# Kernel tuning notes

Hardware: AMD Instinct MI355X
Metric: run time of the kernel (lower is better)

Reference implementation:

```python
import jax, jax.numpy as jnp
import numpy as np

N, E, M, H, D, G, C = 50000, 400000, 4, 400, 3, 128, 10
BN_EPS = 1e-5


def setup_inputs() -> dict:
    key = jax.random.key(0)
    ks = iter(jax.random.split(key, 64))

    def rn(shape, s=0.05):
        return (jax.random.normal(next(ks), shape, jnp.float32) * s)

    inp = {}
    inp['x'] = jax.random.normal(next(ks), (N, M), jnp.float32)
    inp['edge_index'] = jax.random.randint(next(ks), (2, E), 0, N, dtype=jnp.int32)
    inp['batch'] = jnp.sort(jax.random.randint(next(ks), (N,), 0, G, dtype=jnp.int32))
    inp['num_graphs'] = G
    # first GINConv MLP: M -> H -> H -> H
    inp['c0_w1'] = rn((H, M)); inp['c0_b1'] = rn((H,))
    inp['c0_g1'] = jnp.ones((H,), jnp.float32); inp['c0_be1'] = jnp.zeros((H,), jnp.float32)
    inp['c0_w2'] = rn((H, H)); inp['c0_b2'] = rn((H,))
    inp['c0_g2'] = jnp.ones((H,), jnp.float32); inp['c0_be2'] = jnp.zeros((H,), jnp.float32)
    inp['c0_w3'] = rn((H, H)); inp['c0_b3'] = rn((H,))
    # GINConv layers 1..D-1 (stacked): H -> H -> H -> H
    L = D - 1
    inp['cw1'] = rn((L, H, H)); inp['cb1'] = rn((L, H))
    inp['cg1'] = jnp.ones((L, H), jnp.float32); inp['cbe1'] = jnp.zeros((L, H), jnp.float32)
    inp['cw2'] = rn((L, H, H)); inp['cb2'] = rn((L, H))
    inp['cg2'] = jnp.ones((L, H), jnp.float32); inp['cbe2'] = jnp.zeros((L, H), jnp.float32)
    inp['cw3'] = rn((L, H, H)); inp['cb3'] = rn((L, H))
    # readout head
    inp['lin1_w'] = rn((H * D // 2, H * D)); inp['lin1_b'] = rn((H * D // 2,))
    inp['lin2_w'] = rn((C, H * D // 2)); inp['lin2_b'] = rn((C,))
    return inp


def _bn(z, g, b):
    # training-mode BatchNorm1d over nodes (biased variance, eps=1e-5)
    m = z.mean(axis=0)
    v = ((z - m) ** 2).mean(axis=0)
    return (z - m) * jax.lax.rsqrt(v + BN_EPS) * g + b


def _mlp(h, w1, b1, g1, be1, w2, b2, g2, be2, w3, b3):
    # PyG MLP(num_layers=3): Lin->BN->ReLU, Lin->BN->ReLU, Lin (plain last)
    h = jax.nn.relu(_bn(h @ w1.T + b1, g1, be1))
    h = jax.nn.relu(_bn(h @ w2.T + b2, g2, be2))
    return h @ w3.T + b3


def reference(x, edge_index, batch, num_graphs,
              c0_w1, c0_b1, c0_g1, c0_be1, c0_w2, c0_b2, c0_g2, c0_be2, c0_w3, c0_b3,
              cw1, cb1, cg1, cbe1, cw2, cb2, cg2, cbe2, cw3, cb3,
              lin1_w, lin1_b, lin2_w, lin2_b):
    src, dst = edge_index[0], edge_index[1]
    n = x.shape[0]

    def gin_agg(h):
        # eps = -1.0 => (1+eps)*x_i term vanishes; pure neighbor scatter-add
        return jax.ops.segment_sum(h[src], dst, num_segments=n)

    pools = []
    h = _mlp(gin_agg(x), c0_w1, c0_b1, c0_g1, c0_be1,
             c0_w2, c0_b2, c0_g2, c0_be2, c0_w3, c0_b3)
    pools.append(jax.ops.segment_sum(h, batch, num_segments=num_graphs))
    for i in range(D - 1):
        h = _mlp(gin_agg(h), cw1[i], cb1[i], cg1[i], cbe1[i],
                 cw2[i], cb2[i], cg2[i], cbe2[i], cw3[i], cb3[i])
        pools.append(jax.ops.segment_sum(h, batch, num_segments=num_graphs))
    xG = jnp.concatenate(pools, axis=1)                 # [G, D*H]
    z = jax.nn.relu(xG @ lin1_w.T + lin1_b)             # dropout off (eval)
    z = z @ lin2_w.T + lin2_b
    return jax.nn.log_softmax(z, axis=1)
```

## Files before the change

### kernel.cpp

```cpp
#include <hip/hip_runtime.h>
#include <hip/hip_bf16.h>
#include <math.h>
#include <cstdint>

static constexpr int NN = 50000;
static constexpr int NE = 400000;
static constexpr int H  = 400;
static constexpr int NG = 128;
static constexpr int NC = 10;
static constexpr float EPS = 1e-5f;
static constexpr int NB1 = (NN + 255) / 256;
static constexpr int KP  = 416;
static constexpr int SREP = 8;
static constexpr int SSLOT = SREP * 2 * KP;

typedef unsigned short u16;
typedef __attribute__((ext_vector_type(8))) unsigned short u16x8;
typedef __attribute__((ext_vector_type(4))) unsigned short u16x4;
typedef __attribute__((ext_vector_type(8))) short bf16x8;
typedef __attribute__((ext_vector_type(4))) float f32x4;

__device__ __forceinline__ float bf2f(u16 u) {
    return __uint_as_float(((uint32_t)u) << 16);
}
__device__ __forceinline__ u16 f2bf(float f) {
    uint32_t u = __float_as_uint(f);
    return (u16)((u + 0x7FFFu + ((u >> 16) & 1u)) >> 16);
}
__device__ __forceinline__ void gload_lds16(const void* g, void* lds) {
    __builtin_amdgcn_global_load_lds((const __attribute__((address_space(1))) void*)g,
                                     (__attribute__((address_space(3))) void*)lds, 16, 0, 0);
}

__device__ __forceinline__ bf16x8 bnrelu8(bf16x8 a, const float* __restrict__ scp,
                                          const float* __restrict__ shp) {
    union { bf16x8 v; uint32_t u[4]; } in, out;
    in.v = a;
#pragma unroll
    for (int p = 0; p < 4; ++p) {
        float lo = __uint_as_float(in.u[p] << 16);
        float hi = __uint_as_float(in.u[p] & 0xFFFF0000u);
        lo = fmaxf(fmaf(lo, scp[2 * p], shp[2 * p]), 0.f);
        hi = fmaxf(fmaf(hi, scp[2 * p + 1], shp[2 * p + 1]), 0.f);
        asm("v_cvt_pk_bf16_f32 %0, %1, %2" : "=v"(out.u[p]) : "v"(lo), "v"(hi));
    }
    return out.v;
}


__global__ void k_count(const int* __restrict__ dst, int* __restrict__ deg) {
    int e = blockIdx.x * blockDim.x + threadIdx.x;
    if (e < NE) atomicAdd(&deg[dst[e]], 1);
}

__global__ __launch_bounds__(256) void k_scan1(const int* __restrict__ deg,
                                               int* __restrict__ part,
                                               int* __restrict__ btot) {
    __shared__ int sd[256];
    int t = threadIdx.x;
    int i = blockIdx.x * 256 + t;
    int v = (i < NN) ? deg[i] : 0;
    sd[t] = v;
    __syncthreads();
#pragma unroll
    for (int off = 1; off < 256; off <<= 1) {
        int x = (t >= off) ? sd[t - off] : 0;
        __syncthreads();
        sd[t] += x;
        __syncthreads();
    }
    if (i < NN) part[i] = sd[t];
    if (t == 255) btot[blockIdx.x] = sd[255];
}

__global__ __launch_bounds__(256) void k_scan2(int* __restrict__ btot) {
    __shared__ int sd[256];
    int t = threadIdx.x;
    int v = (t < NB1) ? btot[t] : 0;
    sd[t] = v;
    __syncthreads();
#pragma unroll
    for (int off = 1; off < 256; off <<= 1) {
        int x = (t >= off) ? sd[t - off] : 0;
        __syncthreads();
        sd[t] += x;
        __syncthreads();
    }
    if (t < NB1) btot[t] = sd[t];
}

__global__ __launch_bounds__(256) void k_scan3(const int* __restrict__ part,
                                               const int* __restrict__ btot,
                                               const int* __restrict__ deg,
                                               int* __restrict__ rowp,
                                               int* __restrict__ cur) {
    int i = blockIdx.x * 256 + threadIdx.x;
    if (i < NN) {
        int s = part[i] + (blockIdx.x ? btot[blockIdx.x - 1] : 0);
        rowp[i + 1] = s;
        cur[i] = s - deg[i];
    }
    if (i == 0) rowp[0] = 0;
}

__global__ void k_scatter(const int* __restrict__ src, const int* __restrict__ dst,
                          int* __restrict__ cur, int* __restrict__ csrc) {
    int e = blockIdx.x * blockDim.x + threadIdx.x;
    if (e < NE) {
        int d = dst[e];
        int p = atomicAdd(&cur[d], 1);
        csrc[p] = src[e];
    }
}


__global__ __launch_bounds__(256) void k_cntg(const int* __restrict__ batch,
                                              int* __restrict__ cnt) {
    __shared__ int hh[NG];
    int t = threadIdx.x;
    for (int i = t; i < NG; i += 256) hh[i] = 0;
    __syncthreads();
    int n = blockIdx.x * 256 + t;
    if (n < NN) atomicAdd(&hh[batch[n]], 1);
    __syncthreads();
    for (int i = t; i < NG; i += 256)
        if (hh[i]) atomicAdd(&cnt[i], hh[i]);
}


__global__ void k_cvtw3(const float* __restrict__ s0, const float* __restrict__ s1,
                        const float* __restrict__ s2, u16* __restrict__ dst) {
    int i = blockIdx.x * blockDim.x + threadIdx.x;
    if (i >= 3 * 400 * 52) return;
    int rc = i / 52;
    int c8 = (i % 52) * 8;
    u16x8 o = {0, 0, 0, 0, 0, 0, 0, 0};
    if (c8 < 400) {
        int mat = rc / 400, row = rc % 400;
        const float* s = (mat == 0 ? s0 : mat == 1 ? s1 : s2) + (long)row * 400;
        float4 a = *(const float4*)(s + c8);
        float4 b = *(const float4*)(s + c8 + 4);
        o[0] = f2bf(a.x); o[1] = f2bf(a.y); o[2] = f2bf(a.z); o[3] = f2bf(a.w);
        o[4] = f2bf(b.x); o[5] = f2bf(b.y); o[6] = f2bf(b.z); o[7] = f2bf(b.w);
    }
    *(u16x8*)(dst + (long)rc * KP + c8) = o;
}


__global__ __launch_bounds__(256) void k_wmerge(const float* __restrict__ Wa,
                                                const float* __restrict__ Wb,
                                                u16* __restrict__ dst) {
    __shared__ float As[16][68];
    __shared__ float Bs[16][68];
    const int bc = blockIdx.x * 64, bj = blockIdx.y * 64;
    const int t = threadIdx.x;
    const int tx = t & 15, ty = t >> 4;
    float acc[4][4] = {};
    for (int k0 = 0; k0 < 400; k0 += 16) {
        {
            int c = bc + (t >> 2);
            int kq = (t & 3) * 4;
            float4 v = make_float4(0.f, 0.f, 0.f, 0.f);
            if (c < 400) v = *(const float4*)(Wa + (long)c * 400 + k0 + kq);
            As[kq + 0][t >> 2] = v.x; As[kq + 1][t >> 2] = v.y;
            As[kq + 2][t >> 2] = v.z; As[kq + 3][t >> 2] = v.w;
        }
        {
            int k = k0 + (t >> 4);
            int jq = (t & 15) * 4;
            int j = bj + jq;
            float4 v = make_float4(0.f, 0.f, 0.f, 0.f);
            if (j < 400) v = *(const float4*)(Wb + (long)k * 400 + j);
            Bs[t >> 4][jq + 0] = v.x; Bs[t >> 4][jq + 1] = v.y;
            Bs[t >> 4][jq + 2] = v.z; Bs[t >> 4][jq + 3] = v.w;
        }
        __syncthreads();
#pragma unroll
        for (int kk = 0; kk < 16; ++kk) {
            float4 av = *(const float4*)&As[kk][ty * 4];
            float4 bv = *(const float4*)&Bs[kk][tx * 4];
            float a[4] = {av.x, av.y, av.z, av.w};
            float b[4] = {bv.x, bv.y, bv.z, bv.w};
#pragma unroll
            for (int i = 0; i < 4; ++i)
#pragma unroll
                for (int j = 0; j < 4; ++j)
                    acc[i][j] = fmaf(a[i], b[j], acc[i][j]);
        }
        __syncthreads();
    }
#pragma unroll
    for (int i = 0; i < 4; ++i) {
        int c = bc + ty * 4 + i;
        if (c >= 400) continue;
#pragma unroll
        for (int j = 0; j < 4; ++j) {
            int col = bj + tx * 4 + j;
            if (col < KP) dst[(long)c * KP + col] = (col < 400) ? f2bf(acc[i][j]) : 0;
        }
    }
}

__global__ void k_wbias(const float* __restrict__ Wa, const float* __restrict__ b,
                        float* __restrict__ bb) {
    int c = blockIdx.x * blockDim.x + threadIdx.x;
    if (c >= 400) return;
    const float4* wr = (const float4*)(Wa + (long)c * 400);
    const float4* br = (const float4*)b;
    float s0 = 0.f, s1 = 0.f, s2 = 0.f, s3 = 0.f;
    for (int q = 0; q < 100; ++q) {
        float4 a = wr[q], v = br[q];
        s0 = fmaf(a.x, v.x, s0); s1 = fmaf(a.y, v.y, s1);
        s2 = fmaf(a.z, v.z, s2); s3 = fmaf(a.w, v.w, s3);
    }
    bb[c] = s0 + s1 + s2 + s3;
}


__global__ void k_agg0(const float* __restrict__ x, const int* __restrict__ rowp,
                       const int* __restrict__ csrc, float* __restrict__ out) {
    int n = blockIdx.x * blockDim.x + threadIdx.x;
    if (n >= NN) return;
    float4 acc = make_float4(0.f, 0.f, 0.f, 0.f);
    int b = rowp[n], e = rowp[n + 1];
    for (int p = b; p < e; ++p) {
        float4 v = ((const float4*)x)[csrc[p]];
        acc.x += v.x; acc.y += v.y; acc.z += v.z; acc.w += v.w;
    }
    ((float4*)out)[n] = acc;
}

__global__ __launch_bounds__(256) void k_aggH(const u16* __restrict__ h,
                                              const int* __restrict__ rowp,
                                              const int* __restrict__ csrc,
                                              const float* __restrict__ bias,
                                              u16* __restrict__ out) {
    int n = (blockIdx.x << 2) + (threadIdx.x >> 6);
    if (n >= NN) return;
    int l = threadIdx.x & 63;
    if (l >= 50) return;
    float4 b0 = *(const float4*)(bias + l * 8);
    float4 b1 = *(const float4*)(bias + l * 8 + 4);
    float acc[8] = {b0.x, b0.y, b0.z, b0.w, b1.x, b1.y, b1.z, b1.w};
    int b = rowp[n], e = rowp[n + 1];
    for (int p = b; p < e; ++p) {
        const u16* r = h + (long)csrc[p] * H + l * 8;
        u16x8 v = *(const u16x8*)r;
#pragma unroll
        for (int q = 0; q < 8; ++q) acc[q] += bf2f(v[q]);
    }
    u16x8 o;
#pragma unroll
    for (int q = 0; q < 8; ++q) o[q] = f2bf(acc[q]);
    *(u16x8*)(out + (long)n * H + l * 8) = o;
}


__global__ void k_lin0(const float* __restrict__ a4, const float* __restrict__ w,
                       const float* __restrict__ b, u16* __restrict__ out) {
    long i = (long)blockIdx.x * blockDim.x + threadIdx.x;
    if (i >= (long)NN * 100) return;
    int n = (int)(i / 100), q = (int)(i - (long)n * 100);
    int j0 = q * 4;
    float4 av = ((const float4*)a4)[n];
    u16x4 o;
#pragma unroll
    for (int jj = 0; jj < 4; ++jj) {
        float4 wv = ((const float4*)w)[j0 + jj];
        float s = fmaf(av.x, wv.x, fmaf(av.y, wv.y, fmaf(av.z, wv.z, av.w * wv.w)));
        o[jj] = f2bf(s + b[j0 + jj]);
    }
    *(u16x4*)(out + (long)n * H + j0) = o;
}


__global__ __launch_bounds__(256) void k_statsv(const u16* __restrict__ z,
                                                float* __restrict__ stats) {
    __shared__ float ls[800];
    int t = threadIdx.x;
    for (int i = t; i < 800; i += 256) ls[i] = 0.f;
    __syncthreads();
    if (t < 250) {
        int sub = t / 50, seg = t % 50;
        float s[8] = {0, 0, 0, 0, 0, 0, 0, 0};
        float q[8] = {0, 0, 0, 0, 0, 0, 0, 0};
        for (int r = blockIdx.x * 5 + sub; r < NN; r += gridDim.x * 5) {
            u16x8 v = *(const u16x8*)(z + (long)r * H + seg * 8);
#pragma unroll
            for (int j = 0; j < 8; ++j) {
                float f = bf2f(v[j]);
                s[j] += f; q[j] += f * f;
            }
        }
#pragma unroll
        for (int j = 0; j < 8; ++j) {
            atomicAdd(&ls[seg * 8 + j], s[j]);
            atomicAdd(&ls[400 + seg * 8 + j], q[j]);
        }
    }
    __syncthreads();
    const int rep = blockIdx.x & (SREP - 1);
    for (int i = t; i < 800; i += 256) {
        int col = (i < 400) ? i : (i - 400 + KP);
        atomicAdd(&stats[rep * 2 * KP + col], ls[i]);
    }
}


template <bool STATS>
__global__ __launch_bounds__(256) void gemm_mfma(const u16* __restrict__ A,
                                                 const u16* __restrict__ Wp,
                                                 const float* __restrict__ bias,
                                                 const float* __restrict__ bnG,
                                                 const float* __restrict__ bnBe,
                                                 const float* __restrict__ statsIn,
                                                 float* __restrict__ statsOut,
                                                 u16* __restrict__ out, int M) {
    constexpr int BUF = 6656;
    __shared__ u16 lds[3 * BUF];
    __shared__ float sdScale[KP];
    __shared__ float sdShift[KP];
    __shared__ float sst[160];

    const int t = threadIdx.x;
    const int nwg = gridDim.x;
    const int q8 = nwg >> 3, r8 = nwg & 7;
    const int xcd = blockIdx.x & 7, jj = blockIdx.x >> 3;
    const int wgid = (xcd < r8 ? xcd * (q8 + 1) : r8 * (q8 + 1) + (xcd - r8) * q8) + jj;
    const int bm = (wgid / 5) * 128;
    const int bn = (wgid % 5) * 80;
    const int w = t >> 6, l = t & 63;

    for (int j = t; j < KP; j += 256) {
        float s = 0.f, q = 0.f;
#pragma unroll
        for (int r = 0; r < SREP; ++r) {
            s += statsIn[r * 2 * KP + j];
            q += statsIn[r * 2 * KP + KP + j];
        }
        float sc = 0.f, sh = 0.f;
        if (j < H) {
            float m = s / NN;
            float v = fmaxf(q / NN - m * m, 0.f);
            float rs = rsqrtf(v + EPS);
            sc = bnG[j] * rs;
            sh = bnBe[j] - m * sc;
        }
        sdScale[j] = sc;
        sdShift[j] = sh;
    }

    const int srow = l >> 2;
    const int sck  = ((l & 3) ^ ((l >> 3) & 3)) * 8;

    auto stageTile = [&](int b, int kt) {
        u16* dst = lds + b * BUF;
        const int k0 = kt * 32;
        long g0 = (long)bm + w * 16 + srow;
        long g1 = g0 + 64;
        if (g0 > M - 1) g0 = M - 1;
        if (g1 > M - 1) g1 = M - 1;
        gload_lds16(A + g0 * 400 + k0 + sck, dst + w * 512);
        gload_lds16(A + g1 * 400 + k0 + sck, dst + (w + 4) * 512);
        gload_lds16(Wp + (long)(bn + w * 16 + srow) * KP + k0 + sck,
                    dst + 4096 + w * 512);
        gload_lds16(Wp + (long)(bn + 64 + srow) * KP + k0 + sck,
                    dst + 4096 + 4 * 512);
    };

    f32x4 acc[2][5];
#pragma unroll
    for (int i = 0; i < 2; ++i)
#pragma unroll
        for (int c = 0; c < 5; ++c)
            acc[i][c] = (f32x4){0.f, 0.f, 0.f, 0.f};

    const int r16 = l & 15;
    const int cc  = l >> 4;
    const int swz = r16 * 32 + (((cc ^ ((r16 >> 1) & 3))) << 3);

    auto computeTile = [&](int b, int s) {
        const u16* base = lds + b * BUF;
        const u16* ab = base + w * 1024 + swz;
        const u16* bb = base + 4096 + swz;
        bf16x8 fa0 = *(const bf16x8*)ab;
        bf16x8 fa1 = *(const bf16x8*)(ab + 512);
        const int k = s * 32 + cc * 8;
        fa0 = bnrelu8(fa0, sdScale + k, sdShift + k);
        fa1 = bnrelu8(fa1, sdScale + k, sdShift + k);
        __builtin_amdgcn_s_setprio(1);
#pragma unroll
        for (int c = 0; c < 5; ++c) {
            bf16x8 fb = *(const bf16x8*)(bb + c * 512);
            acc[0][c] = __builtin_amdgcn_mfma_f32_16x16x32_bf16(fa0, fb, acc[0][c], 0, 0, 0);
            acc[1][c] = __builtin_amdgcn_mfma_f32_16x16x32_bf16(fa1, fb, acc[1][c], 0, 0, 0);
        }
        __builtin_amdgcn_s_setprio(0);
    };

    stageTile(0, 0);
    stageTile(1, 1);

#pragma unroll 1
    for (int s = 0; s < 12; ++s) {
        asm volatile("s_waitcnt vmcnt(4)" ::: "memory");
        __builtin_amdgcn_s_barrier();
        if (s + 2 < 13) stageTile((s + 2) % 3, s + 2);
        computeTile(s % 3, s);
    }
    asm volatile("s_waitcnt vmcnt(0)" ::: "memory");
    __builtin_amdgcn_s_barrier();
    computeTile(12 % 3, 12);

    u16* tile = lds;
    __syncthreads();
    if (STATS) for (int i = t; i < 160; i += 256) sst[i] = 0.f;
    if (STATS) __syncthreads();

    float ssum[5], sqq[5];
#pragma unroll
    for (int c = 0; c < 5; ++c) { ssum[c] = 0.f; sqq[c] = 0.f; }
#pragma unroll
    for (int i = 0; i < 2; ++i) {
        const int lrow0 = w * 32 + i * 16 + (l >> 4) * 4;
#pragma unroll
        for (int c = 0; c < 5; ++c) {
            const int lcol = c * 16 + (l & 15);
            const float bv = bias[bn + lcol];
#pragma unroll
            for (int r = 0; r < 4; ++r) {
                const int lrow = lrow0 + r;
                float z = acc[i][c][r] + bv;
                tile[lrow * 80 + lcol] = f2bf(z);
                if (STATS && bm + lrow < M) { ssum[c] += z; sqq[c] += z * z; }
            }
        }
    }
    __syncthreads();
#pragma unroll
    for (int j = 0; j < 5; ++j) {
        int chunk = t + j * 256;
        int row = chunk / 10, c8 = chunk % 10;
        if (bm + row < M) {
            u16x8 v = *(const u16x8*)(tile + row * 80 + c8 * 8);
            *(u16x8*)(out + (long)(bm + row) * H + bn + c8 * 8) = v;
        }
    }
    if (STATS) {
        const int rep = wgid & (SREP - 1);
#pragma unroll
        for (int c = 0; c < 5; ++c) {
            ssum[c] += __shfl_xor(ssum[c], 16); ssum[c] += __shfl_xor(ssum[c], 32);
            sqq[c]  += __shfl_xor(sqq[c], 16);  sqq[c]  += __shfl_xor(sqq[c], 32);
        }
        if (l < 16) {
#pragma unroll
            for (int c = 0; c < 5; ++c) {
                atomicAdd(&sst[c * 16 + l], ssum[c]);
                atomicAdd(&sst[80 + c * 16 + l], sqq[c]);
            }
        }
        __syncthreads();
        if (t < 80)       atomicAdd(&statsOut[rep * 2 * KP + bn + t], sst[t]);
        else if (t < 160) atomicAdd(&statsOut[rep * 2 * KP + KP + bn + (t - 80)], sst[t]);
    }
}


__global__ __launch_bounds__(256) void k_poolf(const u16* __restrict__ z,
                                               const float* __restrict__ statsIn,
                                               const float* __restrict__ gw,
                                               const float* __restrict__ be,
                                               const int* __restrict__ batch,
                                               float* __restrict__ pf) {
    __shared__ float sdS[400];
    __shared__ float sdH[400];
    int t = threadIdx.x;
    for (int j = t; j < 400; j += 256) {
        float s = 0.f, q = 0.f;
#pragma unroll
        for (int r = 0; r < SREP; ++r) {
            s += statsIn[r * 2 * KP + j];
            q += statsIn[r * 2 * KP + KP + j];
        }
        float m = s / NN, v = fmaxf(q / NN - m * m, 0.f);
        float rs = rsqrtf(v + EPS);
        float sc = gw[j] * rs;
        sdS[j] = sc;
        sdH[j] = be[j] - m * sc;
    }
    __syncthreads();
    if (t >= 250) return;
    const int sub = t / 50, seg = t % 50;
    float sc[8], sh[8];
#pragma unroll
    for (int q = 0; q < 8; ++q) {
        sc[q] = sdS[seg * 8 + q];
        sh[q] = sdH[seg * 8 + q];
    }
    int rows = (NN + gridDim.x - 1) / gridDim.x;
    int r0 = blockIdx.x * rows;
    int r1 = min(r0 + rows, NN);
    float acc[8] = {0.f, 0.f, 0.f, 0.f, 0.f, 0.f, 0.f, 0.f};
    int gp = -1;
    for (int r = r0 + sub; r < r1; r += 5) {
        int gg = batch[r];
        if (gg != gp) {
            if (gp >= 0) {
#pragma unroll
                for (int q = 0; q < 8; ++q)
                    atomicAdd(&pf[(long)gp * 400 + seg * 8 + q], acc[q]);
            }
#pragma unroll
            for (int q = 0; q < 8; ++q) acc[q] = 0.f;
            gp = gg;
        }
        u16x8 v = *(const u16x8*)(z + (long)r * H + seg * 8);
#pragma unroll
        for (int q = 0; q < 8; ++q)
            acc[q] += fmaxf(fmaf(bf2f(v[q]), sc[q], sh[q]), 0.f);
    }
    if (gp >= 0) {
#pragma unroll
        for (int q = 0; q < 8; ++q)
            atomicAdd(&pf[(long)gp * 400 + seg * 8 + q], acc[q]);
    }
}


__global__ __launch_bounds__(256) void k_poolgemm(const float* __restrict__ pf,
                                                  const float* __restrict__ w30,
                                                  const float* __restrict__ w312,
                                                  const float* __restrict__ b30,
                                                  const float* __restrict__ b312,
                                                  const int* __restrict__ cnt,
                                                  float* __restrict__ pools) {
    __shared__ __align__(16) float xr[400];
    int g = blockIdx.x, L = blockIdx.y, t = threadIdx.x;
    const float* w = (L == 0) ? w30 : w312 + (size_t)(L - 1) * 400 * 400;
    const float* b = (L == 0) ? b30 : b312 + (L - 1) * 400;
    for (int i = t; i < 400; i += 256) xr[i] = pf[((long)L * NG + g) * 400 + i];
    __syncthreads();
    float cg = (float)cnt[g];
    for (int c = t; c < 400; c += 256) {
        const float4* wr = (const float4*)(w + (long)c * 400);
        const float4* xv = (const float4*)xr;
        float s0 = 0.f, s1 = 0.f, s2 = 0.f, s3 = 0.f;
        for (int q = 0; q < 100; ++q) {
            float4 a = xv[q], bb = wr[q];
            s0 = fmaf(a.x, bb.x, s0); s1 = fmaf(a.y, bb.y, s1);
            s2 = fmaf(a.z, bb.z, s2); s3 = fmaf(a.w, bb.w, s3);
        }
        pools[(long)g * 1200 + L * 400 + c] = s0 + s1 + s2 + s3 + cg * b[c];
    }
}


__global__ __launch_bounds__(256) void k_lin1(const float* __restrict__ pools,
                                              const float* __restrict__ w1,
                                              const float* __restrict__ b1,
                                              float* __restrict__ zz) {
    __shared__ __align__(16) float xg[8][1200];
    const int bandj = blockIdx.x * 40;
    const int g0 = blockIdx.y * 8;
    const int t = threadIdx.x;
    for (int i = t; i < 9600; i += 256)
        xg[i / 1200][i % 1200] = pools[(long)(g0 + i / 1200) * 1200 + (i % 1200)];
    __syncthreads();
    const int wv = t >> 6, l = t & 63;
    for (int jj = wv; jj < 40; jj += 4) {
        const int j = bandj + jj;
        const float4* wr = (const float4*)(w1 + (long)j * 1200);
        float s[8] = {0.f, 0.f, 0.f, 0.f, 0.f, 0.f, 0.f, 0.f};
        for (int q = l; q < 300; q += 64) {
            float4 wq = wr[q];
#pragma unroll
            for (int g = 0; g < 8; ++g) {
                float4 xv = *(const float4*)&xg[g][q * 4];
                s[g] = fmaf(wq.x, xv.x, s[g]);
                s[g] = fmaf(wq.y, xv.y, s[g]);
                s[g] = fmaf(wq.z, xv.z, s[g]);
                s[g] = fmaf(wq.w, xv.w, s[g]);
            }
        }
#pragma unroll
        for (int g = 0; g < 8; ++g)
#pragma unroll
            for (int o = 32; o; o >>= 1) s[g] += __shfl_xor(s[g], o);
        if (l == 0) {
            const float bj = b1[j];
#pragma unroll
            for (int g = 0; g < 8; ++g)
                zz[(long)(g0 + g) * 600 + j] = fmaxf(s[g] + bj, 0.f);
        }
    }
}

__global__ __launch_bounds__(64) void k_lin2(const float* __restrict__ zz,
                                             const float* __restrict__ w2,
                                             const float* __restrict__ b2,
                                             float* __restrict__ out) {
    int g = blockIdx.x;
    int l = threadIdx.x;
    float p[NC];
#pragma unroll
    for (int c = 0; c < NC; ++c) p[c] = 0.f;
    for (int k = l; k < 600; k += 64) {
        float zv = zz[(long)g * 600 + k];
#pragma unroll
        for (int c = 0; c < NC; ++c) p[c] = fmaf(zv, w2[c * 600 + k], p[c]);
    }
#pragma unroll
    for (int c = 0; c < NC; ++c)
#pragma unroll
        for (int o = 32; o; o >>= 1) p[c] += __shfl_xor(p[c], o);
    if (l == 0) {
        float lg[NC];
        float mx = -1e30f;
#pragma unroll
        for (int c = 0; c < NC; ++c) { lg[c] = p[c] + b2[c]; mx = fmaxf(mx, lg[c]); }
        float se = 0.f;
#pragma unroll
        for (int c = 0; c < NC; ++c) se += expf(lg[c] - mx);
        float lse = logf(se);
#pragma unroll
        for (int c = 0; c < NC; ++c) out[(long)g * NC + c] = lg[c] - mx - lse;
    }
}


extern "C" void kernel_launch(void* const* d_in, const int* in_sizes, int n_in,
                              void* d_out, int out_size, void* d_ws, size_t ws_size,
                              hipStream_t stream) {
    const float* x      = (const float*)d_in[0];
    const int*   ei     = (const int*)d_in[1];
    const int*   batch  = (const int*)d_in[2];
    const float* c0_w1  = (const float*)d_in[4];
    const float* c0_b1  = (const float*)d_in[5];
    const float* c0_g1  = (const float*)d_in[6];
    const float* c0_be1 = (const float*)d_in[7];
    const float* c0_w2  = (const float*)d_in[8];
    const float* c0_b2  = (const float*)d_in[9];
    const float* c0_g2  = (const float*)d_in[10];
    const float* c0_be2 = (const float*)d_in[11];
    const float* c0_w3  = (const float*)d_in[12];
    const float* c0_b3  = (const float*)d_in[13];
    const float* cw1    = (const float*)d_in[14];
    const float* cb1    = (const float*)d_in[15];
    const float* cg1    = (const float*)d_in[16];
    const float* cbe1   = (const float*)d_in[17];
    const float* cw2    = (const float*)d_in[18];
    const float* cb2    = (const float*)d_in[19];
    const float* cg2    = (const float*)d_in[20];
    const float* cbe2   = (const float*)d_in[21];
    const float* cw3    = (const float*)d_in[22];
    const float* cb3    = (const float*)d_in[23];
    const float* lin1_w = (const float*)d_in[24];
    const float* lin1_b = (const float*)d_in[25];
    const float* lin2_w = (const float*)d_in[26];
    const float* lin2_b = (const float*)d_in[27];

    const int* src = ei;
    const int* dst = ei + NE;

    char* ws = (char*)d_ws;
    size_t off = 0;
    auto alloc = [&](size_t bytes) {
        void* p = ws + off;
        off += (bytes + 255) & ~(size_t)255;
        return p;
    };
    u16*   bufh   = (u16*)alloc((size_t)NN * H * 2 + 128);
    u16*   bufa   = (u16*)alloc((size_t)NN * H * 2 + 128);
    float* agg0   = (float*)alloc((size_t)NN * 4 * 4);
    float* statsA = (float*)alloc((size_t)6 * SSLOT * 4);
    float* pf     = (float*)alloc((size_t)3 * NG * 400 * 4);
    float* pools  = (float*)alloc((size_t)NG * 3 * H * 4);
    float* zz     = (float*)alloc((size_t)NG * 600 * 4);
    float* bb1    = (float*)alloc(400 * 4);
    float* bb2    = (float*)alloc(400 * 4);
    u16*   wpad   = (u16*)alloc((size_t)5 * 400 * KP * 2);
    int*   deg    = (int*)alloc((size_t)NN * 4);
    int*   rowp   = (int*)alloc((size_t)(NN + 1) * 4);
    int*   cur    = (int*)alloc((size_t)NN * 4);
    int*   csrc   = (int*)alloc((size_t)NE * 4);
    int*   part   = (int*)alloc((size_t)NN * 4);
    int*   btot   = (int*)alloc((size_t)NB1 * 4);
    int*   cnt    = (int*)alloc((size_t)NG * 4);

    auto wp   = [&](int mat) { return wpad + (size_t)mat * 400 * KP; };
    auto slot = [&](int i)   { return statsA + (size_t)i * SSLOT; };

    hipMemsetAsync(deg, 0, (size_t)NN * 4, stream);
    hipMemsetAsync(statsA, 0, (size_t)6 * SSLOT * 4, stream);
    hipMemsetAsync(pf, 0, (size_t)3 * NG * 400 * 4, stream);
    hipMemsetAsync(cnt, 0, (size_t)NG * 4, stream);

    k_cvtw3<<<(3 * 400 * 52 + 255) / 256, 256, 0, stream>>>(c0_w2, cw2, cw2 + 160000, wpad);
    dim3 gm(7, 7);
    k_wmerge<<<gm, 256, 0, stream>>>(cw1, c0_w3, wp(3));
    k_wmerge<<<gm, 256, 0, stream>>>(cw1 + 160000, cw3, wp(4));
    k_wbias<<<2, 256, 0, stream>>>(cw1, c0_b3, bb1);
    k_wbias<<<2, 256, 0, stream>>>(cw1 + 160000, cb3, bb2);

    k_count<<<(NE + 255) / 256, 256, 0, stream>>>(dst, deg);
    k_scan1<<<NB1, 256, 0, stream>>>(deg, part, btot);
    k_scan2<<<1, 256, 0, stream>>>(btot);
    k_scan3<<<NB1, 256, 0, stream>>>(part, btot, deg, rowp, cur);
    k_scatter<<<(NE + 255) / 256, 256, 0, stream>>>(src, dst, cur, csrc);
    k_cntg<<<NB1, 256, 0, stream>>>(batch, cnt);

    const int ngemm = ((NN + 127) / 128) * 5;

    k_agg0<<<(NN + 255) / 256, 256, 0, stream>>>(x, rowp, csrc, agg0);
    k_lin0<<<(int)(((long)NN * 100 + 255) / 256), 256, 0, stream>>>(agg0, c0_w1, c0_b1, bufh);
    k_statsv<<<256, 256, 0, stream>>>(bufh, slot(0));
    gemm_mfma<true><<<ngemm, 256, 0, stream>>>(bufh, wp(0), c0_b2, c0_g1, c0_be1,
                                               slot(0), slot(1), bufa, NN);
    gemm_mfma<false><<<ngemm, 256, 0, stream>>>(bufa, wp(3), bb1, c0_g2, c0_be2,
                                                slot(1), nullptr, bufh, NN);
    k_poolf<<<512, 256, 0, stream>>>(bufa, slot(1), c0_g2, c0_be2, batch, pf);

    k_aggH<<<(NN + 3) / 4, 256, 0, stream>>>(bufh, rowp, csrc, cb1, bufa);
    k_statsv<<<256, 256, 0, stream>>>(bufa, slot(2));
    gemm_mfma<true><<<ngemm, 256, 0, stream>>>(bufa, wp(1), cb2, cg1, cbe1,
                                               slot(2), slot(3), bufh, NN);
    gemm_mfma<false><<<ngemm, 256, 0, stream>>>(bufh, wp(4), bb2, cg2, cbe2,
                                                slot(3), nullptr, bufa, NN);
    k_poolf<<<512, 256, 0, stream>>>(bufh, slot(3), cg2, cbe2, batch, pf + (size_t)NG * 400);

    k_aggH<<<(NN + 3) / 4, 256, 0, stream>>>(bufa, rowp, csrc, cb1 + 400, bufh);
    k_statsv<<<256, 256, 0, stream>>>(bufh, slot(4));
    gemm_mfma<true><<<ngemm, 256, 0, stream>>>(bufh, wp(2), cb2 + 400, cg1 + 400,
                                               cbe1 + 400, slot(4), slot(5), bufa, NN);
    k_poolf<<<512, 256, 0, stream>>>(bufa, slot(5), cg2 + 400, cbe2 + 400, batch,
                                     pf + (size_t)2 * NG * 400);

    dim3 gp(NG, 3);
    k_poolgemm<<<gp, 256, 0, stream>>>(pf, c0_w3, cw3, c0_b3, cb3, cnt, pools);
    dim3 gl1(15, 16);
    k_lin1<<<gl1, 256, 0, stream>>>(pools, lin1_w, lin1_b, zz);
    k_lin2<<<NG, 64, 0, stream>>>(zz, lin2_w, lin2_b, (float*)d_out);
}
```

Baseline: 825.4 us.

## Fuse BatchNorm statistics into aggregation kernels and derive layer-0 stats analytically

Removes the separate k_statsv passes over the 50000x400 activations. The aggH kernel now accumulates per-column sum and sum-of-squares while it aggregates, handling 4 nodes per wave, and pushes them to the stats slots through LDS and global atomics. For the first layer, k_agg0 reduces the first and second moments of the 4-wide aggregated input, and a small kernel maps them through the 4->400 linear layer to get the BN statistics exactly. The trade-off is fp32 pre-rounding stats instead of bf16-rounded ones, possible cancellation in the analytic variance, and fewer blocks with serial per-wave node loops in aggH.

After: 851.5 us. +3.2%, slower.

```diff
diff --git a/kernel.cpp b/kernel.cpp
--- a/kernel.cpp
+++ b/kernel.cpp
@@ -217,42 +217,111 @@
 }
 
 
-__global__ void k_agg0(const float* __restrict__ x, const int* __restrict__ rowp,
-                       const int* __restrict__ csrc, float* __restrict__ out) {
+__global__ __launch_bounds__(256) void k_agg0(const float* __restrict__ x,
+                                              const int* __restrict__ rowp,
+                                              const int* __restrict__ csrc,
+                                              float* __restrict__ out,
+                                              float* __restrict__ mom) {
+    __shared__ float ws[4][14];
     int n = blockIdx.x * blockDim.x + threadIdx.x;
-    if (n >= NN) return;
     float4 acc = make_float4(0.f, 0.f, 0.f, 0.f);
-    int b = rowp[n], e = rowp[n + 1];
-    for (int p = b; p < e; ++p) {
-        float4 v = ((const float4*)x)[csrc[p]];
-        acc.x += v.x; acc.y += v.y; acc.z += v.z; acc.w += v.w;
-    }
-    ((float4*)out)[n] = acc;
-}
+    if (n < NN) {
+        int b = rowp[n], e = rowp[n + 1];
+        for (int p = b; p < e; ++p) {
+            float4 v = ((const float4*)x)[csrc[p]];
+            acc.x += v.x; acc.y += v.y; acc.z += v.z; acc.w += v.w;
+        }
+        ((float4*)out)[n] = acc;
+    }
+    float mv[14] = {acc.x, acc.y, acc.z, acc.w,
+                    acc.x * acc.x, acc.x * acc.y, acc.x * acc.z, acc.x * acc.w,
+                    acc.y * acc.y, acc.y * acc.z, acc.y * acc.w,
+                    acc.z * acc.z, acc.z * acc.w, acc.w * acc.w};
+    int wv = threadIdx.x >> 6, l = threadIdx.x & 63;
+#pragma unroll
+    for (int i = 0; i < 14; ++i) {
+        float s = mv[i];
+#pragma unroll
+        for (int o = 32; o; o >>= 1) s += __shfl_xor(s, o);
+        if (l == 0) ws[wv][i] = s;
+    }
+    __syncthreads();
+    if (threadIdx.x < 14) {
+        float s = ws[0][threadIdx.x] + ws[1][threadIdx.x] + ws[2][threadIdx.x] + ws[3][threadIdx.x];
+        atomicAdd(&mom[threadIdx.x], s);
+    }
+}
+
+__global__ void k_stats0(const float* __restrict__ mom, const float* __restrict__ w1,
+                         const float* __restrict__ b1, float* __restrict__ slot0) {
+    int j = blockIdx.x * blockDim.x + threadIdx.x;
+    if (j >= 400) return;
+    float4 w = ((const float4*)w1)[j];
+    float dot = w.x * mom[0] + w.y * mom[1] + w.z * mom[2] + w.w * mom[3];
+    float quad = w.x * w.x * mom[4] + 2.f * w.x * w.y * mom[5] + 2.f * w.x * w.z * mom[6]
+               + 2.f * w.x * w.w * mom[7] + w.y * w.y * mom[8] + 2.f * w.y * w.z * mom[9]
+               + 2.f * w.y * w.w * mom[10] + w.z * w.z * mom[11] + 2.f * w.z * w.w * mom[12]
+               + w.w * w.w * mom[13];
+    float b = b1[j];
+    slot0[j] = dot + (float)NN * b;
+    slot0[KP + j] = quad + 2.f * b * dot + (float)NN * b * b;
+}
+
 
 __global__ __launch_bounds__(256) void k_aggH(const u16* __restrict__ h,
                                               const int* __restrict__ rowp,
                                               const int* __restrict__ csrc,
                                               const float* __restrict__ bias,
-                                              u16* __restrict__ out) {
-    int n = (blockIdx.x << 2) + (threadIdx.x >> 6);
-    if (n >= NN) return;
-    int l = threadIdx.x & 63;
-    if (l >= 50) return;
-    float4 b0 = *(const float4*)(bias + l * 8);
-    float4 b1 = *(const float4*)(bias + l * 8 + 4);
-    float acc[8] = {b0.x, b0.y, b0.z, b0.w, b1.x, b1.y, b1.z, b1.w};
-    int b = rowp[n], e = rowp[n + 1];
-    for (int p = b; p < e; ++p) {
-        const u16* r = h + (long)csrc[p] * H + l * 8;
-        u16x8 v = *(const u16x8*)r;
-#pragma unroll
-        for (int q = 0; q < 8; ++q) acc[q] += bf2f(v[q]);
-    }
-    u16x8 o;
-#pragma unroll
-    for (int q = 0; q < 8; ++q) o[q] = f2bf(acc[q]);
-    *(u16x8*)(out + (long)n * H + l * 8) = o;
+                                              u16* __restrict__ out,
+                                              float* __restrict__ stats) {
+    __shared__ float ls[800];
+    const int t = threadIdx.x;
+    for (int i = t; i < 800; i += 256) ls[i] = 0.f;
+    __syncthreads();
+    const int wv = t >> 6, l = t & 63;
+    const bool active = (l < 50);
+    float4 b0 = make_float4(0.f, 0.f, 0.f, 0.f), b1v = b0;
+    if (active) {
+        b0  = *(const float4*)(bias + l * 8);
+        b1v = *(const float4*)(bias + l * 8 + 4);
+    }
+    float ssum[8] = {0.f, 0.f, 0.f, 0.f, 0.f, 0.f, 0.f, 0.f};
+    float ssq[8]  = {0.f, 0.f, 0.f, 0.f, 0.f, 0.f, 0.f, 0.f};
+    const int n0 = blockIdx.x * 16 + wv * 4;
+#pragma unroll 1
+    for (int ni = 0; ni < 4; ++ni) {
+        const int n = n0 + ni;
+        if (active && n < NN) {
+            float acc[8] = {b0.x, b0.y, b0.z, b0.w, b1v.x, b1v.y, b1v.z, b1v.w};
+            int b = rowp[n], e = rowp[n + 1];
+            for (int p = b; p < e; ++p) {
+                u16x8 v = *(const u16x8*)(h + (long)csrc[p] * H + l * 8);
+#pragma unroll
+                for (int q = 0; q < 8; ++q) acc[q] += bf2f(v[q]);
+            }
+            u16x8 o;
+#pragma unroll
+            for (int q = 0; q < 8; ++q) {
+                o[q] = f2bf(acc[q]);
+                ssum[q] += acc[q];
+                ssq[q]  += acc[q] * acc[q];
+            }
+            *(u16x8*)(out + (long)n * H + l * 8) = o;
+        }
+    }
+    if (active) {
+#pragma unroll
+        for (int q = 0; q < 8; ++q) {
+            atomicAdd(&ls[l * 8 + q], ssum[q]);
+            atomicAdd(&ls[400 + l * 8 + q], ssq[q]);
+        }
+    }
+    __syncthreads();
+    const int rep = blockIdx.x & (SREP - 1);
+    for (int i = t; i < 800; i += 256) {
+        int col = (i < 400) ? i : (i - 400 + KP);
+        atomicAdd(&stats[rep * 2 * KP + col], ls[i]);
+    }
 }
 
 
@@ -271,39 +340,6 @@
         o[jj] = f2bf(s + b[j0 + jj]);
     }
     *(u16x4*)(out + (long)n * H + j0) = o;
-}
-
-
-__global__ __launch_bounds__(256) void k_statsv(const u16* __restrict__ z,
-                                                float* __restrict__ stats) {
-    __shared__ float ls[800];
-    int t = threadIdx.x;
-    for (int i = t; i < 800; i += 256) ls[i] = 0.f;
-    __syncthreads();
-    if (t < 250) {
-        int sub = t / 50, seg = t % 50;
-        float s[8] = {0, 0, 0, 0, 0, 0, 0, 0};
-        float q[8] = {0, 0, 0, 0, 0, 0, 0, 0};
-        for (int r = blockIdx.x * 5 + sub; r < NN; r += gridDim.x * 5) {
-            u16x8 v = *(const u16x8*)(z + (long)r * H + seg * 8);
-#pragma unroll
-            for (int j = 0; j < 8; ++j) {
-                float f = bf2f(v[j]);
-                s[j] += f; q[j] += f * f;
-            }
-        }
-#pragma unroll
-        for (int j = 0; j < 8; ++j) {
-            atomicAdd(&ls[seg * 8 + j], s[j]);
-            atomicAdd(&ls[400 + seg * 8 + j], q[j]);
-        }
-    }
-    __syncthreads();
-    const int rep = blockIdx.x & (SREP - 1);
-    for (int i = t; i < 800; i += 256) {
-        int col = (i < 400) ? i : (i - 400 + KP);
-        atomicAdd(&stats[rep * 2 * KP + col], ls[i]);
-    }
 }
 
 
@@ -674,6 +710,7 @@
     u16*   bufa   = (u16*)alloc((size_t)NN * H * 2 + 128);
     float* agg0   = (float*)alloc((size_t)NN * 4 * 4);
     float* statsA = (float*)alloc((size_t)6 * SSLOT * 4);
+    float* mom    = (float*)alloc(14 * 4);
     float* pf     = (float*)alloc((size_t)3 * NG * 400 * 4);
     float* pools  = (float*)alloc((size_t)NG * 3 * H * 4);
     float* zz     = (float*)alloc((size_t)NG * 600 * 4);
@@ -693,6 +730,7 @@
 
     hipMemsetAsync(deg, 0, (size_t)NN * 4, stream);
     hipMemsetAsync(statsA, 0, (size_t)6 * SSLOT * 4, stream);
+    hipMemsetAsync(mom, 0, 14 * 4, stream);
     hipMemsetAsync(pf, 0, (size_t)3 * NG * 400 * 4, stream);
     hipMemsetAsync(cnt, 0, (size_t)NG * 4, stream);
 
@@ -712,25 +750,23 @@
 
     const int ngemm = ((NN + 127) / 128) * 5;
 
-    k_agg0<<<(NN + 255) / 256, 256, 0, stream>>>(x, rowp, csrc, agg0);
+    k_agg0<<<NB1, 256, 0, stream>>>(x, rowp, csrc, agg0, mom);
+    k_stats0<<<2, 256, 0, stream>>>(mom, c0_w1, c0_b1, slot(0));
     k_lin0<<<(int)(((long)NN * 100 + 255) / 256), 256, 0, stream>>>(agg0, c0_w1, c0_b1, bufh);
-    k_statsv<<<256, 256, 0, stream>>>(bufh, slot(0));
     gemm_mfma<true><<<ngemm, 256, 0, stream>>>(bufh, wp(0), c0_b2, c0_g1, c0_be1,
                                                slot(0), slot(1), bufa, NN);
     gemm_mfma<false><<<ngemm, 256, 0, stream>>>(bufa, wp(3), bb1, c0_g2, c0_be2,
                                                 slot(1), nullptr, bufh, NN);
     k_poolf<<<512, 256, 0, stream>>>(bufa, slot(1), c0_g2, c0_be2, batch, pf);
 
-    k_aggH<<<(NN + 3) / 4, 256, 0, stream>>>(bufh, rowp, csrc, cb1, bufa);
-    k_statsv<<<256, 256, 0, stream>>>(bufa, slot(2));
+    k_aggH<<<(NN + 15) / 16, 256, 0, stream>>>(bufh, rowp, csrc, cb1, bufa, slot(2));
     gemm_mfma<true><<<ngemm, 256, 0, stream>>>(bufa, wp(1), cb2, cg1, cbe1,
                                                slot(2), slot(3), bufh, NN);
     gemm_mfma<false><<<ngemm, 256, 0, stream>>>(bufh, wp(4), bb2, cg2, cbe2,
                                                 slot(3), nullptr, bufa, NN);
     k_poolf<<<512, 256, 0, stream>>>(bufh, slot(3), cg2, cbe2, batch, pf + (size_t)NG * 400);
 
-    k_aggH<<<(NN + 3) / 4, 256, 0, stream>>>(bufa, rowp, csrc, cb1 + 400, bufh);
-    k_statsv<<<256, 256, 0, stream>>>(bufh, slot(4));
+    k_aggH<<<(NN + 15) / 16, 256, 0, stream>>>(bufa, rowp, csrc, cb1 + 400, bufh, slot(4));
     gemm_mfma<true><<<ngemm, 256, 0, stream>>>(bufh, wp(2), cb2 + 400, cg1 + 400,
                                                cbe1 + 400, slot(4), slot(5), bufa, NN);
     k_poolf<<<512, 256, 0, stream>>>(bufa, slot(5), cg2 + 400, cbe2 + 400, batch,
```

## Derive first-layer BatchNorm stats analytically from input moments instead of a full pass

Applied to the files above, without the earlier changes.

The first aggregation kernel now also block-reduces the 4 sums and 10 second-order products of the 4-wide aggregated input and accumulates them with atomics. A small kernel then computes each of the 400 channel sums and sums of squares of the first linear layer's output from those moments and the weights. This replaces the statistics pass that read the whole 50000x400 bf16 activation buffer. The stats now come from fp32 values rather than the bf16-rounded stored ones. The variance now rests on fp32 moment sums, which adds some cancellation and atomic-ordering risk.

Result: no change. 812.8 us (-1.5%).

```diff
diff --git a/kernel.cpp b/kernel.cpp
--- a/kernel.cpp
+++ b/kernel.cpp
@@ -217,18 +217,56 @@
 }
 
 
-__global__ void k_agg0(const float* __restrict__ x, const int* __restrict__ rowp,
-                       const int* __restrict__ csrc, float* __restrict__ out) {
+__global__ __launch_bounds__(256) void k_agg0(const float* __restrict__ x,
+                                              const int* __restrict__ rowp,
+                                              const int* __restrict__ csrc,
+                                              float* __restrict__ out,
+                                              float* __restrict__ mom) {
+    __shared__ float ws[4][14];
     int n = blockIdx.x * blockDim.x + threadIdx.x;
-    if (n >= NN) return;
     float4 acc = make_float4(0.f, 0.f, 0.f, 0.f);
-    int b = rowp[n], e = rowp[n + 1];
-    for (int p = b; p < e; ++p) {
-        float4 v = ((const float4*)x)[csrc[p]];
-        acc.x += v.x; acc.y += v.y; acc.z += v.z; acc.w += v.w;
-    }
-    ((float4*)out)[n] = acc;
-}
+    if (n < NN) {
+        int b = rowp[n], e = rowp[n + 1];
+        for (int p = b; p < e; ++p) {
+            float4 v = ((const float4*)x)[csrc[p]];
+            acc.x += v.x; acc.y += v.y; acc.z += v.z; acc.w += v.w;
+        }
+        ((float4*)out)[n] = acc;
+    }
+    float mv[14] = {acc.x, acc.y, acc.z, acc.w,
+                    acc.x * acc.x, acc.x * acc.y, acc.x * acc.z, acc.x * acc.w,
+                    acc.y * acc.y, acc.y * acc.z, acc.y * acc.w,
+                    acc.z * acc.z, acc.z * acc.w, acc.w * acc.w};
+    int wv = threadIdx.x >> 6, l = threadIdx.x & 63;
+#pragma unroll
+    for (int i = 0; i < 14; ++i) {
+        float s = mv[i];
+#pragma unroll
+        for (int o = 32; o; o >>= 1) s += __shfl_xor(s, o);
+        if (l == 0) ws[wv][i] = s;
+    }
+    __syncthreads();
+    if (threadIdx.x < 14) {
+        float s = ws[0][threadIdx.x] + ws[1][threadIdx.x] + ws[2][threadIdx.x] + ws[3][threadIdx.x];
+        atomicAdd(&mom[threadIdx.x], s);
+    }
+}
+
+__global__ void k_stats0(const float* __restrict__ mom, const float* __restrict__ w1,
+                         const float* __restrict__ b1, float* __restrict__ slot0) {
+    int j = blockIdx.x * blockDim.x + threadIdx.x;
+    if (j >= 400) return;
+    float4 w = ((const float4*)w1)[j];
+    float dot = w.x * mom[0] + w.y * mom[1] + w.z * mom[2] + w.w * mom[3];
+    float quad = w.x * w.x * mom[4] + 2.f * w.x * w.y * mom[5] + 2.f * w.x * w.z * mom[6]
+               + 2.f * w.x * w.w * mom[7] + w.y * w.y * mom[8] + 2.f * w.y * w.z * mom[9]
+               + 2.f * w.y * w.w * mom[10] + w.z * w.z * mom[11] + 2.f * w.z * w.w * mom[12]
+               + w.w * w.w * mom[13];
+    float b = b1[j];
+    slot0[j] = dot + (float)NN * b;
+    slot0[KP + j] = quad + 2.f * b * dot + (float)NN * b * b;
+}
+
 
 __global__ __launch_bounds__(256) void k_aggH(const u16* __restrict__ h,
                                               const int* __restrict__ rowp,
@@ -674,6 +712,7 @@
     u16*   bufa   = (u16*)alloc((size_t)NN * H * 2 + 128);
     float* agg0   = (float*)alloc((size_t)NN * 4 * 4);
     float* statsA = (float*)alloc((size_t)6 * SSLOT * 4);
+    float* mom    = (float*)alloc(14 * 4);
     float* pf     = (float*)alloc((size_t)3 * NG * 400 * 4);
     float* pools  = (float*)alloc((size_t)NG * 3 * H * 4);
     float* zz     = (float*)alloc((size_t)NG * 600 * 4);
@@ -693,6 +732,7 @@
 
     hipMemsetAsync(deg, 0, (size_t)NN * 4, stream);
     hipMemsetAsync(statsA, 0, (size_t)6 * SSLOT * 4, stream);
+    hipMemsetAsync(mom, 0, 14 * 4, stream);
     hipMemsetAsync(pf, 0, (size_t)3 * NG * 400 * 4, stream);
     hipMemsetAsync(cnt, 0, (size_t)NG * 4, stream);
 
@@ -712,9 +752,9 @@
 
     const int ngemm = ((NN + 127) / 128) * 5;
 
-    k_agg0<<<(NN + 255) / 256, 256, 0, stream>>>(x, rowp, csrc, agg0);
+    k_agg0<<<NB1, 256, 0, stream>>>(x, rowp, csrc, agg0, mom);
+    k_stats0<<<2, 256, 0, stream>>>(mom, c0_w1, c0_b1, slot(0));
     k_lin0<<<(int)(((long)NN * 100 + 255) / 256), 256, 0, stream>>>(agg0, c0_w1, c0_b1, bufh);
-    k_statsv<<<256, 256, 0, stream>>>(bufh, slot(0));
     gemm_mfma<true><<<ngemm, 256, 0, stream>>>(bufh, wp(0), c0_b2, c0_g1, c0_be1,
                                                slot(0), slot(1), bufa, NN);
     gemm_mfma<false><<<ngemm, 256, 0, stream>>>(bufa, wp(3), bb1, c0_g2, c0_be2,
```
